# Performance work log

Hardware: AMD Instinct MI355X
Metric: run time of the kernel (lower is better)

Reference implementation:

```python
import jax, jax.numpy as jnp
import numpy as np

B, T, D_MODEL, HEAD_DIM = 4, 4096, 1024, 2


def setup_inputs() -> dict:
    key = jax.random.key(0)
    kx, kq, kk, kv = jax.random.split(key, 4)
    x = jax.random.normal(kx, (B, T, D_MODEL), dtype=jnp.float32)
    # nn.Linear weights: (out_features, in_features), applied as x @ W.T
    s_qk = 1.0 / np.sqrt(D_MODEL)
    W_Q = jax.random.uniform(kq, (HEAD_DIM, D_MODEL), minval=-s_qk, maxval=s_qk, dtype=jnp.float32)
    W_K = jax.random.uniform(kk, (HEAD_DIM, D_MODEL), minval=-s_qk, maxval=s_qk, dtype=jnp.float32)
    W_V = jax.random.uniform(kv, (D_MODEL, D_MODEL), minval=-s_qk, maxval=s_qk, dtype=jnp.float32)
    # strict upper-triangular True = masked (future positions)
    causal_mask = jnp.triu(jnp.ones((T, T), dtype=bool), k=1)[None, :, :]
    return {"x": x, "W_Q": W_Q, "W_K": W_K, "W_V": W_V, "causal_mask": causal_mask}


def reference(x, W_Q, W_K, W_V, causal_mask):
    # x: (B, T, d_model)
    Q = jnp.einsum('btd,hd->bth', x, W_Q)   # (B, T, head_dim)
    K = jnp.einsum('bsd,hd->bsh', x, W_K)   # (B, S, head_dim)
    V = jnp.einsum('bsd,ed->bse', x, W_V)   # (B, S, d_model)
    scores = jnp.einsum('bth,bsh->bts', Q, K)              # (B, T, S)
    scores = jnp.where(causal_mask, -jnp.inf, scores)
    max_idx = jnp.argmax(scores, axis=-1)                  # (B, T)
    # one-hot scatter + bmm in the original == hard gather of V rows
    out = jnp.take_along_axis(V, max_idx[..., None], axis=1)  # (B, T, d_model)
    return out
```

## Files before the change

### kernel.cpp

```cpp
#include <hip/hip_runtime.h>
#include <math.h>

#define TT 4096
#define DM 1024
#define BB 4
#define BT (BB * TT)
#define SENTINEL 0x7fffffff


__device__ __forceinline__ float dot4(const float4 a, const float4 b) {
    return a.x * b.x + a.y * b.y + a.z * b.z + a.w * b.w;
}

__global__ __launch_bounds__(256) void qk_kernel(const float* __restrict__ x,
                                                 const float* __restrict__ wq,
                                                 const float* __restrict__ wk,
                                                 float* __restrict__ Q,
                                                 float* __restrict__ K,
                                                 int* __restrict__ rep,
                                                 int* __restrict__ cnt) {
    __shared__ float4 wqs0[256], wqs1[256], wks0[256], wks1[256];
    const int tid = threadIdx.x;
    const int row0 = blockIdx.x * 4;

    wqs0[tid] = ((const float4*)(wq))[tid];
    wqs1[tid] = ((const float4*)(wq + DM))[tid];
    wks0[tid] = ((const float4*)(wk))[tid];
    wks1[tid] = ((const float4*)(wk + DM))[tid];

    if (tid < 4) rep[row0 + tid] = SENTINEL;
    if (blockIdx.x == 0 && tid == 4) cnt[0] = 0;
    __syncthreads();

    const int wave = tid >> 6, lane = tid & 63;
    const int row = row0 + wave;
    const float4* xr = (const float4*)(x + (size_t)row * DM);

    float s0 = 0.f, s1 = 0.f, s2 = 0.f, s3 = 0.f;
    #pragma unroll
    for (int j = 0; j < 4; ++j) {
        const float4 xv = xr[j * 64 + lane];
        s0 += dot4(xv, wqs0[j * 64 + lane]);
        s1 += dot4(xv, wqs1[j * 64 + lane]);
        s2 += dot4(xv, wks0[j * 64 + lane]);
        s3 += dot4(xv, wks1[j * 64 + lane]);
    }
    #pragma unroll
    for (int off = 32; off > 0; off >>= 1) {
        s0 += __shfl_down(s0, off);
        s1 += __shfl_down(s1, off);
        s2 += __shfl_down(s2, off);
        s3 += __shfl_down(s3, off);
    }
    if (lane == 0) {
        ((float2*)Q)[row] = make_float2(s0, s1);
        ((float2*)K)[row] = make_float2(s2, s3);
    }
}

__global__ __launch_bounds__(256) void argmax_kernel(const float* __restrict__ Q,
                                                     const float* __restrict__ K,
                                                     int* __restrict__ idx,
                                                     int* __restrict__ rep,
                                                     int* __restrict__ list,
                                                     int* __restrict__ cnt) {
    __shared__ float2 ks[TT];
    const int b  = blockIdx.x >> 10;
    const int tg = blockIdx.x & 1023;
    const int tid = threadIdx.x;
    const int nfill = tg * 4 + 4;

    const float2* kb = (const float2*)(K + (size_t)b * TT * 2);
    for (int i = tid; i < nfill; i += 256) ks[i] = kb[i];
    __syncthreads();

    const int wave = tid >> 6, lane = tid & 63;
    const int t = tg * 4 + wave;
    const float2 q = ((const float2*)Q)[b * TT + t];
    const float4* kp = (const float4*)ks;

    float best = -INFINITY;
    int bi = 0x7fffffff;
    int p = lane;
    while (2 * (p + 64) + 1 <= t) {
        const float4 a = kp[p];
        const float4 c = kp[p + 64];
        const float c0 = q.x * a.x + q.y * a.y;
        const float c1 = q.x * a.z + q.y * a.w;
        const float c2 = q.x * c.x + q.y * c.y;
        const float c3 = q.x * c.z + q.y * c.w;
        if (c0 > best) { best = c0; bi = 2 * p; }
        if (c1 > best) { best = c1; bi = 2 * p + 1; }
        if (c2 > best) { best = c2; bi = 2 * (p + 64); }
        if (c3 > best) { best = c3; bi = 2 * (p + 64) + 1; }
        p += 128;
    }
    while (2 * p <= t) {
        const float4 a = kp[p];
        const float c0 = q.x * a.x + q.y * a.y;
        if (c0 > best) { best = c0; bi = 2 * p; }
        if (2 * p + 1 <= t) {
            const float c1 = q.x * a.z + q.y * a.w;
            if (c1 > best) { best = c1; bi = 2 * p + 1; }
        }
        p += 64;
    }
    #pragma unroll
    for (int off = 32; off > 0; off >>= 1) {
        const float ov = __shfl_down(best, off);
        const int   oi = __shfl_down(bi, off);
        if (ov > best || (ov == best && oi < bi)) { best = ov; bi = oi; }
    }
    if (lane == 0) {
        idx[b * TT + t] = bi;
        const int old = atomicMin(&rep[b * TT + bi], t);
        if (old == SENTINEL) {
            const int pp = atomicAdd(cnt, 1);
            list[pp] = b * TT + bi;
        }
    }
}

__global__ __launch_bounds__(256) void vrow_kernel(const float* __restrict__ x,
                                                   const float* __restrict__ wv,
                                                   const int* __restrict__ rep,
                                                   const int* __restrict__ list,
                                                   const int* __restrict__ cnt,
                                                   float* __restrict__ out) {
    const int tid = threadIdx.x, wave = tid >> 6, lane = tid & 63;
    const int slice = blockIdx.x >> 4;
    const int usub  = blockIdx.x & 15;
    const int e0 = slice * 16 + wave * 4;

    float4 w[4][4];
    #pragma unroll
    for (int r = 0; r < 4; ++r) {
        const float4* wr = (const float4*)(wv + (size_t)(e0 + r) * DM);
        #pragma unroll
        for (int j = 0; j < 4; ++j) w[r][j] = wr[j * 64 + lane];
    }

    const int n = cnt[0];
    for (int li = usub; li < n; li += 16) {
        const int bs = list[li];
        const int b  = bs >> 12;
        const int r  = rep[bs];
        const float4* xr = (const float4*)(x + (size_t)bs * DM);
        float4 xv[4];
        #pragma unroll
        for (int j = 0; j < 4; ++j) xv[j] = xr[j * 64 + lane];

        float s0 = 0.f, s1 = 0.f, s2 = 0.f, s3 = 0.f;
        #pragma unroll
        for (int j = 0; j < 4; ++j) {
            s0 += dot4(w[0][j], xv[j]);
            s1 += dot4(w[1][j], xv[j]);
            s2 += dot4(w[2][j], xv[j]);
            s3 += dot4(w[3][j], xv[j]);
        }
        #pragma unroll
        for (int off = 32; off > 0; off >>= 1) {
            s0 += __shfl_down(s0, off);
            s1 += __shfl_down(s1, off);
            s2 += __shfl_down(s2, off);
            s3 += __shfl_down(s3, off);
        }
        if (lane == 0)
            *(float4*)(out + ((size_t)(b * TT + r)) * DM + e0) = make_float4(s0, s1, s2, s3);
    }
}

__global__ __launch_bounds__(256) void gather_kernel(const int* __restrict__ idx,
                                                     const int* __restrict__ rep,
                                                     float* __restrict__ out) {
    const int bt = blockIdx.x;
    const int b = bt >> 12, t = bt & (TT - 1);
    const int s = idx[bt];
    const int r = rep[b * TT + s];
    if (r == t) return;
    const float4* src = (const float4*)(out + ((size_t)(b * TT + r)) * DM);
    float4* dst = (float4*)(out + (size_t)bt * DM);
    dst[threadIdx.x] = src[threadIdx.x];
}

extern "C" void kernel_launch(void* const* d_in, const int* in_sizes, int n_in,
                              void* d_out, int out_size, void* d_ws, size_t ws_size,
                              hipStream_t stream) {
    const float* x  = (const float*)d_in[0];
    const float* wq = (const float*)d_in[1];
    const float* wk = (const float*)d_in[2];
    const float* wv = (const float*)d_in[3];
    float* out = (float*)d_out;

    char* ws = (char*)d_ws;
    float* Q    = (float*)(ws);
    float* K    = (float*)(ws + 131072);
    int*   idx  = (int*)  (ws + 262144);
    int*   rep  = (int*)  (ws + 327680);
    int*   list = (int*)  (ws + 393216);
    int*   cnt  = (int*)  (ws + 458752);

    qk_kernel<<<BT / 4, 256, 0, stream>>>(x, wq, wk, Q, K, rep, cnt);
    argmax_kernel<<<4096, 256, 0, stream>>>(Q, K, idx, rep, list, cnt);
    vrow_kernel<<<1024, 256, 0, stream>>>(x, wv, rep, list, cnt, out);
    gather_kernel<<<BT, 256, 0, stream>>>(idx, rep, out);
}
```

Measured before the change: 215.0 us.

## Fuse four stages into one persistent cooperative kernel with grid syncs

Replaces the four separate kernel launches (QK projection, causal argmax, V-row compute, gather) with a single cooperative persistent kernel that separates the stages with grid.sync. Argmax work is load-balanced by pairing triangular tiles (tg and 1023-tg) across batches within each block. This removes launch gaps and evens out the causal triangle, but it caps the grid at the occupancy-derived size and adds grid-wide barrier costs. The shared K staging is reloaded per slot with extra __syncthreads. It falls back to the old launches if the cooperative launch fails.

New measurement: 394.2 us. 83.3% more time.

```diff
diff --git a/kernel.cpp b/kernel.cpp
--- a/kernel.cpp
+++ b/kernel.cpp
@@ -1,5 +1,8 @@
 #include <hip/hip_runtime.h>
+#include <hip/hip_cooperative_groups.h>
 #include <math.h>
+
+namespace cg = cooperative_groups;
 
 #define TT 4096
 #define DM 1024
@@ -10,6 +13,173 @@
 
 __device__ __forceinline__ float dot4(const float4 a, const float4 b) {
     return a.x * b.x + a.y * b.y + a.z * b.z + a.w * b.w;
+}
+
+__global__ __launch_bounds__(256, 4) void fused_kernel(
+    const float* __restrict__ x, const float* __restrict__ wq,
+    const float* __restrict__ wk, const float* __restrict__ wv,
+    float* __restrict__ Q, float* __restrict__ K,
+    int* __restrict__ idx, int* __restrict__ rep,
+    int* __restrict__ list, int* __restrict__ cnt,
+    float* __restrict__ out)
+{
+    __shared__ union {
+        float4 w[4][256];
+        float2 ks[TT];
+    } sm;
+
+    const int tid  = threadIdx.x;
+    const int bid  = blockIdx.x;
+    const int nblk = gridDim.x;
+    const int wave = tid >> 6, lane = tid & 63;
+    cg::grid_group grid = cg::this_grid();
+
+    sm.w[0][tid] = ((const float4*)(wq))[tid];
+    sm.w[1][tid] = ((const float4*)(wq + DM))[tid];
+    sm.w[2][tid] = ((const float4*)(wk))[tid];
+    sm.w[3][tid] = ((const float4*)(wk + DM))[tid];
+    for (int i = bid * 256 + tid; i < BT; i += nblk * 256) rep[i] = SENTINEL;
+    if (bid == 0 && tid == 0) cnt[0] = 0;
+    __syncthreads();
+
+    for (int vb = bid; vb < BT / 4; vb += nblk) {
+        const int row = vb * 4 + wave;
+        const float4* xr = (const float4*)(x + (size_t)row * DM);
+        float s0 = 0.f, s1 = 0.f, s2 = 0.f, s3 = 0.f;
+        #pragma unroll
+        for (int j = 0; j < 4; ++j) {
+            const float4 xv = xr[j * 64 + lane];
+            s0 += dot4(xv, sm.w[0][j * 64 + lane]);
+            s1 += dot4(xv, sm.w[1][j * 64 + lane]);
+            s2 += dot4(xv, sm.w[2][j * 64 + lane]);
+            s3 += dot4(xv, sm.w[3][j * 64 + lane]);
+        }
+        #pragma unroll
+        for (int off = 32; off > 0; off >>= 1) {
+            s0 += __shfl_down(s0, off);
+            s1 += __shfl_down(s1, off);
+            s2 += __shfl_down(s2, off);
+            s3 += __shfl_down(s3, off);
+        }
+        if (lane == 0) {
+            ((float2*)Q)[row] = make_float2(s0, s1);
+            ((float2*)K)[row] = make_float2(s2, s3);
+        }
+    }
+
+    grid.sync();
+
+    for (int i = bid; i < 1024; i += nblk) {
+        #pragma unroll
+        for (int slot = 0; slot < 4; ++slot) {
+            const int b  = slot;
+            const int tg = (slot & 1) ? (1023 - i) : i;
+            const int nfill = tg * 4 + 4;
+            const float2* kb = (const float2*)K + (size_t)b * TT;
+            for (int k2 = tid; k2 < nfill; k2 += 256) sm.ks[k2] = kb[k2];
+            __syncthreads();
+
+            const int t = tg * 4 + wave;
+            const float2 q = ((const float2*)Q)[b * TT + t];
+            const float4* kp = (const float4*)sm.ks;
+
+            float best = -INFINITY;
+            int bi = SENTINEL;
+            int p = lane;
+            while (2 * (p + 64) + 1 <= t) {
+                const float4 a = kp[p];
+                const float4 c = kp[p + 64];
+                const float c0 = q.x * a.x + q.y * a.y;
+                const float c1 = q.x * a.z + q.y * a.w;
+                const float c2 = q.x * c.x + q.y * c.y;
+                const float c3 = q.x * c.z + q.y * c.w;
+                if (c0 > best) { best = c0; bi = 2 * p; }
+                if (c1 > best) { best = c1; bi = 2 * p + 1; }
+                if (c2 > best) { best = c2; bi = 2 * (p + 64); }
+                if (c3 > best) { best = c3; bi = 2 * (p + 64) + 1; }
+                p += 128;
+            }
+            while (2 * p <= t) {
+                const float4 a = kp[p];
+                const float c0 = q.x * a.x + q.y * a.y;
+                if (c0 > best) { best = c0; bi = 2 * p; }
+                if (2 * p + 1 <= t) {
+                    const float c1 = q.x * a.z + q.y * a.w;
+                    if (c1 > best) { best = c1; bi = 2 * p + 1; }
+                }
+                p += 64;
+            }
+            #pragma unroll
+            for (int off = 32; off > 0; off >>= 1) {
+                const float ov = __shfl_down(best, off);
+                const int   oi = __shfl_down(bi, off);
+                if (ov > best || (ov == best && oi < bi)) { best = ov; bi = oi; }
+            }
+            if (lane == 0) {
+                idx[b * TT + t] = bi;
+                const int old = atomicMin(&rep[b * TT + bi], t);
+                if (old == SENTINEL) {
+                    const int pp = atomicAdd(cnt, 1);
+                    list[pp] = b * TT + bi;
+                }
+            }
+            __syncthreads();
+        }
+    }
+
+    grid.sync();
+
+    const int n = cnt[0];
+    for (int vb = bid; vb < 1024; vb += nblk) {
+        const int slice = vb >> 4;
+        const int usub  = vb & 15;
+        const int e0 = slice * 16 + wave * 4;
+        float4 w[4][4];
+        #pragma unroll
+        for (int r = 0; r < 4; ++r) {
+            const float4* wr = (const float4*)(wv + (size_t)(e0 + r) * DM);
+            #pragma unroll
+            for (int j = 0; j < 4; ++j) w[r][j] = wr[j * 64 + lane];
+        }
+        for (int li = usub; li < n; li += 16) {
+            const int bs = list[li];
+            const int b  = bs >> 12;
+            const int r  = rep[bs];
+            const float4* xr = (const float4*)(x + (size_t)bs * DM);
+            float4 xv[4];
+            #pragma unroll
+            for (int j = 0; j < 4; ++j) xv[j] = xr[j * 64 + lane];
+            float s0 = 0.f, s1 = 0.f, s2 = 0.f, s3 = 0.f;
+            #pragma unroll
+            for (int j = 0; j < 4; ++j) {
+                s0 += dot4(w[0][j], xv[j]);
+                s1 += dot4(w[1][j], xv[j]);
+                s2 += dot4(w[2][j], xv[j]);
+                s3 += dot4(w[3][j], xv[j]);
+            }
+            #pragma unroll
+            for (int off = 32; off > 0; off >>= 1) {
+                s0 += __shfl_down(s0, off);
+                s1 += __shfl_down(s1, off);
+                s2 += __shfl_down(s2, off);
+                s3 += __shfl_down(s3, off);
+            }
+            if (lane == 0)
+                *(float4*)(out + ((size_t)(b * TT + r)) * DM + e0) = make_float4(s0, s1, s2, s3);
+        }
+    }
+
+    grid.sync();
+
+    for (int bt = bid; bt < BT; bt += nblk) {
+        const int b = bt >> 12, t = bt & (TT - 1);
+        const int s = idx[bt];
+        const int r = rep[b * TT + s];
+        if (r == t) continue;
+        const float4* src = (const float4*)(out + ((size_t)(b * TT + r)) * DM);
+        float4* dst = (float4*)(out + (size_t)bt * DM);
+        dst[tid] = src[tid];
+    }
 }
 
 __global__ __launch_bounds__(256) void qk_kernel(const float* __restrict__ x,
@@ -200,8 +370,34 @@
     int*   list = (int*)  (ws + 393216);
     int*   cnt  = (int*)  (ws + 458752);
 
-    qk_kernel<<<BT / 4, 256, 0, stream>>>(x, wq, wk, Q, K, rep, cnt);
-    argmax_kernel<<<4096, 256, 0, stream>>>(Q, K, idx, rep, list, cnt);
-    vrow_kernel<<<1024, 256, 0, stream>>>(x, wv, rep, list, cnt, out);
-    gather_kernel<<<BT, 256, 0, stream>>>(idx, rep, out);
-}
+    static int coop_grid = -2;
+    if (coop_grid == -2) {
+        int occ = 0;
+        if (hipOccupancyMaxActiveBlocksPerMultiprocessor(
+                &occ, (const void*)fused_kernel, 256, 0) == hipSuccess && occ > 0) {
+            coop_grid = occ * 256;
+            if (coop_grid > 1024) coop_grid = 1024;
+        } else {
+            coop_grid = -1;
+        }
+    }
+
+    bool done = false;
+    if (coop_grid > 0) {
+        void* args[] = {(void*)&x, (void*)&wq, (void*)&wk, (void*)&wv,
+                        (void*)&Q, (void*)&K, (void*)&idx, (void*)&rep,
+                        (void*)&list, (void*)&cnt, (void*)&out};
+        hipError_t e = hipLaunchCooperativeKernel((const void*)fused_kernel,
+                                                  dim3(coop_grid), dim3(256),
+                                                  args, 0, stream);
+        if (e == hipSuccess) done = true;
+        else coop_grid = -1;
+    }
+
+    if (!done) {
+        qk_kernel<<<BT / 4, 256, 0, stream>>>(x, wq, wk, Q, K, rep, cnt);
+        argmax_kernel<<<4096, 256, 0, stream>>>(Q, K, idx, rep, list, cnt);
+        vrow_kernel<<<1024, 256, 0, stream>>>(x, wv, rep, list, cnt, out);
+        gather_kernel<<<BT, 256, 0, stream>>>(idx, rep, out);
+    }
+}
```

## Pair triangular argmax rows per block and batch rows in qk and gather kernels

Applied to the files above, without the earlier changes.

The argmax kernel now has each block handle two row groups, j and 1023-j, so every block does a similar amount of causal work. It loads the longer K prefix once into shared memory with float4 copies. The qk kernel processes 8 rows per block to amortize the shared weight loads. The gather kernel copies one row per wave, 4 rows per block, instead of one row per block. These changes target load imbalance and per-block launch overhead, at the cost of fewer blocks and less parallelism.

New measurement: 212.4 us (median of 2 runs). Within noise of the previous version (-1.2%).

```diff
diff --git a/kernel.cpp b/kernel.cpp
--- a/kernel.cpp
+++ b/kernel.cpp
@@ -19,42 +19,46 @@
                                                  float* __restrict__ K,
                                                  int* __restrict__ rep,
                                                  int* __restrict__ cnt) {
-    __shared__ float4 wqs0[256], wqs1[256], wks0[256], wks1[256];
+    __shared__ float4 ws[4][256];
     const int tid = threadIdx.x;
-    const int row0 = blockIdx.x * 4;
-
-    wqs0[tid] = ((const float4*)(wq))[tid];
-    wqs1[tid] = ((const float4*)(wq + DM))[tid];
-    wks0[tid] = ((const float4*)(wk))[tid];
-    wks1[tid] = ((const float4*)(wk + DM))[tid];
-
-    if (tid < 4) rep[row0 + tid] = SENTINEL;
-    if (blockIdx.x == 0 && tid == 4) cnt[0] = 0;
+    const int row0 = blockIdx.x * 8;
+
+    ws[0][tid] = ((const float4*)(wq))[tid];
+    ws[1][tid] = ((const float4*)(wq + DM))[tid];
+    ws[2][tid] = ((const float4*)(wk))[tid];
+    ws[3][tid] = ((const float4*)(wk + DM))[tid];
+
+    if (tid < 8) rep[row0 + tid] = SENTINEL;
+    if (blockIdx.x == 0 && tid == 8) cnt[0] = 0;
     __syncthreads();
 
     const int wave = tid >> 6, lane = tid & 63;
-    const int row = row0 + wave;
-    const float4* xr = (const float4*)(x + (size_t)row * DM);
-
-    float s0 = 0.f, s1 = 0.f, s2 = 0.f, s3 = 0.f;
-    #pragma unroll
-    for (int j = 0; j < 4; ++j) {
-        const float4 xv = xr[j * 64 + lane];
-        s0 += dot4(xv, wqs0[j * 64 + lane]);
-        s1 += dot4(xv, wqs1[j * 64 + lane]);
-        s2 += dot4(xv, wks0[j * 64 + lane]);
-        s3 += dot4(xv, wks1[j * 64 + lane]);
-    }
-    #pragma unroll
-    for (int off = 32; off > 0; off >>= 1) {
-        s0 += __shfl_down(s0, off);
-        s1 += __shfl_down(s1, off);
-        s2 += __shfl_down(s2, off);
-        s3 += __shfl_down(s3, off);
-    }
-    if (lane == 0) {
-        ((float2*)Q)[row] = make_float2(s0, s1);
-        ((float2*)K)[row] = make_float2(s2, s3);
+
+    #pragma unroll
+    for (int g = 0; g < 2; ++g) {
+        const int row = row0 + g * 4 + wave;
+        const float4* xr = (const float4*)(x + (size_t)row * DM);
+
+        float s0 = 0.f, s1 = 0.f, s2 = 0.f, s3 = 0.f;
+        #pragma unroll
+        for (int j = 0; j < 4; ++j) {
+            const float4 xv = xr[j * 64 + lane];
+            s0 += dot4(xv, ws[0][j * 64 + lane]);
+            s1 += dot4(xv, ws[1][j * 64 + lane]);
+            s2 += dot4(xv, ws[2][j * 64 + lane]);
+            s3 += dot4(xv, ws[3][j * 64 + lane]);
+        }
+        #pragma unroll
+        for (int off = 32; off > 0; off >>= 1) {
+            s0 += __shfl_down(s0, off);
+            s1 += __shfl_down(s1, off);
+            s2 += __shfl_down(s2, off);
+            s3 += __shfl_down(s3, off);
+        }
+        if (lane == 0) {
+            ((float2*)Q)[row] = make_float2(s0, s1);
+            ((float2*)K)[row] = make_float2(s2, s3);
+        }
     }
 }
 
@@ -65,58 +69,64 @@
                                                      int* __restrict__ list,
                                                      int* __restrict__ cnt) {
     __shared__ float2 ks[TT];
-    const int b  = blockIdx.x >> 10;
-    const int tg = blockIdx.x & 1023;
+    const int b = blockIdx.x >> 9;
+    const int j = blockIdx.x & 511;
     const int tid = threadIdx.x;
-    const int nfill = tg * 4 + 4;
-
-    const float2* kb = (const float2*)(K + (size_t)b * TT * 2);
-    for (int i = tid; i < nfill; i += 256) ks[i] = kb[i];
+
+    const int nfill4 = (((1023 - j) * 4 + 4) >> 1);
+    const float4* kb4 = (const float4*)(K + (size_t)b * TT * 2);
+    float4* ks4 = (float4*)ks;
+    for (int i = tid; i < nfill4; i += 256) ks4[i] = kb4[i];
     __syncthreads();
 
     const int wave = tid >> 6, lane = tid & 63;
-    const int t = tg * 4 + wave;
-    const float2 q = ((const float2*)Q)[b * TT + t];
     const float4* kp = (const float4*)ks;
 
-    float best = -INFINITY;
-    int bi = 0x7fffffff;
-    int p = lane;
-    while (2 * (p + 64) + 1 <= t) {
-        const float4 a = kp[p];
-        const float4 c = kp[p + 64];
-        const float c0 = q.x * a.x + q.y * a.y;
-        const float c1 = q.x * a.z + q.y * a.w;
-        const float c2 = q.x * c.x + q.y * c.y;
-        const float c3 = q.x * c.z + q.y * c.w;
-        if (c0 > best) { best = c0; bi = 2 * p; }
-        if (c1 > best) { best = c1; bi = 2 * p + 1; }
-        if (c2 > best) { best = c2; bi = 2 * (p + 64); }
-        if (c3 > best) { best = c3; bi = 2 * (p + 64) + 1; }
-        p += 128;
-    }
-    while (2 * p <= t) {
-        const float4 a = kp[p];
-        const float c0 = q.x * a.x + q.y * a.y;
-        if (c0 > best) { best = c0; bi = 2 * p; }
-        if (2 * p + 1 <= t) {
+    #pragma unroll
+    for (int u = 0; u < 2; ++u) {
+        const int tg = u ? j : (1023 - j);
+        const int t = tg * 4 + wave;
+        const float2 q = ((const float2*)Q)[b * TT + t];
+
+        float best = -INFINITY;
+        int bi = SENTINEL;
+        int p = lane;
+        while (2 * (p + 64) + 1 <= t) {
+            const float4 a = kp[p];
+            const float4 c = kp[p + 64];
+            const float c0 = q.x * a.x + q.y * a.y;
             const float c1 = q.x * a.z + q.y * a.w;
+            const float c2 = q.x * c.x + q.y * c.y;
+            const float c3 = q.x * c.z + q.y * c.w;
+            if (c0 > best) { best = c0; bi = 2 * p; }
             if (c1 > best) { best = c1; bi = 2 * p + 1; }
-        }
-        p += 64;
-    }
-    #pragma unroll
-    for (int off = 32; off > 0; off >>= 1) {
-        const float ov = __shfl_down(best, off);
-        const int   oi = __shfl_down(bi, off);
-        if (ov > best || (ov == best && oi < bi)) { best = ov; bi = oi; }
-    }
-    if (lane == 0) {
-        idx[b * TT + t] = bi;
-        const int old = atomicMin(&rep[b * TT + bi], t);
-        if (old == SENTINEL) {
-            const int pp = atomicAdd(cnt, 1);
-            list[pp] = b * TT + bi;
+            if (c2 > best) { best = c2; bi = 2 * (p + 64); }
+            if (c3 > best) { best = c3; bi = 2 * (p + 64) + 1; }
+            p += 128;
+        }
+        while (2 * p <= t) {
+            const float4 a = kp[p];
+            const float c0 = q.x * a.x + q.y * a.y;
+            if (c0 > best) { best = c0; bi = 2 * p; }
+            if (2 * p + 1 <= t) {
+                const float c1 = q.x * a.z + q.y * a.w;
+                if (c1 > best) { best = c1; bi = 2 * p + 1; }
+            }
+            p += 64;
+        }
+        #pragma unroll
+        for (int off = 32; off > 0; off >>= 1) {
+            const float ov = __shfl_down(best, off);
+            const int   oi = __shfl_down(bi, off);
+            if (ov > best || (ov == best && oi < bi)) { best = ov; bi = oi; }
+        }
+        if (lane == 0) {
+            idx[b * TT + t] = bi;
+            const int old = atomicMin(&rep[b * TT + bi], t);
+            if (old == SENTINEL) {
+                const int pp = atomicAdd(cnt, 1);
+                list[pp] = b * TT + bi;
+            }
         }
     }
 }
@@ -173,14 +183,16 @@
 __global__ __launch_bounds__(256) void gather_kernel(const int* __restrict__ idx,
                                                      const int* __restrict__ rep,
                                                      float* __restrict__ out) {
-    const int bt = blockIdx.x;
+    const int tid = threadIdx.x, wave = tid >> 6, lane = tid & 63;
+    const int bt = blockIdx.x * 4 + wave;
     const int b = bt >> 12, t = bt & (TT - 1);
     const int s = idx[bt];
     const int r = rep[b * TT + s];
     if (r == t) return;
     const float4* src = (const float4*)(out + ((size_t)(b * TT + r)) * DM);
     float4* dst = (float4*)(out + (size_t)bt * DM);
-    dst[threadIdx.x] = src[threadIdx.x];
+    #pragma unroll
+    for (int k = 0; k < 4; ++k) dst[k * 64 + lane] = src[k * 64 + lane];
 }
 
 extern "C" void kernel_launch(void* const* d_in, const int* in_sizes, int n_in,
@@ -200,8 +212,8 @@
     int*   list = (int*)  (ws + 393216);
     int*   cnt  = (int*)  (ws + 458752);
 
-    qk_kernel<<<BT / 4, 256, 0, stream>>>(x, wq, wk, Q, K, rep, cnt);
-    argmax_kernel<<<4096, 256, 0, stream>>>(Q, K, idx, rep, list, cnt);
+    qk_kernel<<<BT / 8, 256, 0, stream>>>(x, wq, wk, Q, K, rep, cnt);
+    argmax_kernel<<<BB * 512, 256, 0, stream>>>(Q, K, idx, rep, list, cnt);
     vrow_kernel<<<1024, 256, 0, stream>>>(x, wv, rep, list, cnt, out);
-    gather_kernel<<<BT, 256, 0, stream>>>(idx, rep, out);
-}
+    gather_kernel<<<BT / 4, 256, 0, stream>>>(idx, rep, out);
+}
```
